# Performance work log

Hardware: AMD Instinct MI355X
Metric: run time of the kernel (lower is better)

## Reference

```python
import jax, jax.numpy as jnp
import numpy as np

HEADS = 8  # init heads


def setup_inputs() -> dict:
    key = jax.random.key(0)
    k1, k2, k3, k4 = jax.random.split(key, 4)
    B, C, L = 32, 512, 32  # batch, dim, lateral_size
    x = jax.random.normal(k1, (B, C, L, L), dtype=jnp.float32)
    # 1x1 conv with no bias == per-pixel matmul; store as [3*dim, dim]
    qkv_w = jax.random.normal(k2, (3 * C, C), dtype=jnp.float32) * (1.0 / np.sqrt(C))
    h_pos = jax.random.normal(k3, (L, 1, C), dtype=jnp.float32) * 0.02
    w_pos = jax.random.normal(k4, (1, L, C), dtype=jnp.float32) * 0.02
    return {"x": x, "qkv_w": qkv_w, "h_pos": h_pos, "w_pos": w_pos}


def reference(x, qkv_w, h_pos, w_pos):
    B, C, H, W = x.shape
    p = HEADS
    d = C // p
    n = H * W
    # QKV 1x1 conv -> [B, 3C, H, W]
    qkv = jnp.einsum('oc,bchw->bohw', qkv_w, x)
    q, k, v = jnp.split(qkv, 3, axis=1)
    # 'b (p d) h w -> b p (h w) d'
    def to_heads(t):
        return t.reshape(B, p, d, H, W).transpose(0, 1, 3, 4, 2).reshape(B, p, n, d)
    q, k, v = to_heads(q), to_heads(k), to_heads(v)
    # relative pos: [H,1,C] + [1,W,C] -> [H,W,C]; 'h w (p d) -> p (h w) d'
    rp = (h_pos + w_pos).reshape(H, W, p, d).transpose(2, 0, 1, 3).reshape(p, n, d)
    # content-position + content-content scores: [B, p, n, n]
    scores = jnp.einsum('bpnd,pmd->bpnm', q, rp) + jnp.einsum('bpnd,bpmd->bpnm', q, k)
    attn = jax.nn.softmax(scores, axis=-1)
    out = jnp.einsum('bpnm,bpmd->bpnd', attn, v)
    # 'b p (h w) d -> b (p d) h w'
    return out.reshape(B, p, H, W, d).transpose(0, 1, 4, 2, 3).reshape(B, C, H, W)
```

## Files before the change

### kernel.cpp

```cpp
#include <hip/hip_runtime.h>
#include <hip/hip_bf16.h>
#include <hip/hip_fp16.h>

#define HEADS 8
#define BB 32
#define CC 512
#define NN 1024
#define DD 64

typedef _Float16 f16;
typedef __attribute__((ext_vector_type(8))) _Float16 f16x8;
typedef __attribute__((ext_vector_type(4))) _Float16 f16x4;
typedef __attribute__((ext_vector_type(2))) __fp16 hf16x2;
typedef __attribute__((ext_vector_type(4))) float f32x4;

__global__ __launch_bounds__(256) void wconv(
    const float* __restrict__ W, f16* __restrict__ Wh)
{
    const size_t i = ((size_t)blockIdx.x * 256 + threadIdx.x) * 8;
    float4 a = *(const float4*)(W + i);
    float4 b = *(const float4*)(W + i + 4);
    f16x8 h = {(f16)a.x, (f16)a.y, (f16)a.z, (f16)a.w,
               (f16)b.x, (f16)b.y, (f16)b.z, (f16)b.w};
    *(f16x8*)(Wh + i) = h;
}

__global__ __launch_bounds__(256) void prep_x(
    const float* __restrict__ x, f16* __restrict__ xt)
{
    __shared__ f16 T[64][65];
    const int tid = threadIdx.x;
    const int c0 = blockIdx.x * 64;
    const int m0 = blockIdx.y * 64;
    const int b  = blockIdx.z;
    const float* xb = x + (size_t)b * CC * NN;

    const int m_l = tid & 63, c_l = tid >> 6;
    #pragma unroll
    for (int s = 0; s < 16; ++s) {
        const int cr = s * 4 + c_l;
        T[cr][m_l] = (f16)xb[(size_t)(c0 + cr) * NN + m0 + m_l];
    }
    __syncthreads();
    const int m_r = tid >> 2, cq = (tid & 3) * 16;
    f16 buf[16];
    #pragma unroll
    for (int j = 0; j < 16; ++j) buf[j] = T[cq + j][m_r];
    f16* dst = xt + ((size_t)b * NN + m0 + m_r) * CC + c0 + cq;
    *(f16x8*)dst       = *(f16x8*)&buf[0];
    *(f16x8*)(dst + 8) = *(f16x8*)&buf[8];
}

#define QST 72

__global__ __launch_bounds__(256) void qkv_mfma(
    const f16*  __restrict__ xt,
    const f16*  __restrict__ Wh,
    const float* __restrict__ h_pos,
    const float* __restrict__ w_pos,
    f16* __restrict__ Qh, f16* __restrict__ Kh, f16* __restrict__ Vt)
{
    __shared__ f16 Xs[128 * QST];
    __shared__ f16 Ws[128 * QST];

    const int tid  = threadIdx.x;
    const int wave = tid >> 6, lane = tid & 63;
    const int ln = lane & 15, quad = lane >> 4;
    const int o0  = blockIdx.x * 128;
    const int mg0 = blockIdx.y * 128;
    const int mw = (wave & 1) * 64, ow = (wave >> 1) * 64;

    f32x4 acc[4][4];
    #pragma unroll
    for (int ia = 0; ia < 4; ++ia)
        #pragma unroll
        for (int ib = 0; ib < 4; ++ib) acc[ia][ib] = (f32x4){0.f, 0.f, 0.f, 0.f};

    const int srow = tid >> 1;
    const int ssub = (tid & 1) * 32;

    for (int ct = 0; ct < 8; ++ct) {
        const int c0 = ct * 64;
        __syncthreads();
        {
            const f16* xg = xt + (size_t)(mg0 + srow) * CC + c0 + ssub;
            const f16* wg = Wh + (size_t)(o0 + srow) * CC + c0 + ssub;
            #pragma unroll
            for (int i = 0; i < 4; ++i) {
                *(f16x8*)&Xs[srow * QST + ssub + i * 8] = *(const f16x8*)(xg + i * 8);
                *(f16x8*)&Ws[srow * QST + ssub + i * 8] = *(const f16x8*)(wg + i * 8);
            }
        }
        __syncthreads();
        #pragma unroll
        for (int ks = 0; ks < 2; ++ks) {
            f16x8 a[4], bf[4];
            #pragma unroll
            for (int f = 0; f < 4; ++f) {
                a[f]  = *(const f16x8*)&Xs[(mw + f * 16 + ln) * QST + ks * 32 + quad * 8];
                bf[f] = *(const f16x8*)&Ws[(ow + f * 16 + ln) * QST + ks * 32 + quad * 8];
            }
            #pragma unroll
            for (int ia = 0; ia < 4; ++ia)
                #pragma unroll
                for (int ib = 0; ib < 4; ++ib)
                    acc[ia][ib] = __builtin_amdgcn_mfma_f32_16x16x32_f16(
                        a[ia], bf[ib], acc[ia][ib], 0, 0, 0);
        }
    }

    const int region = o0 >> 9;
    const int ob = o0 + ow;
    const int p  = (ob >> 6) & 7;
    const int b  = mg0 >> 10;
    const int n0 = (mg0 & 1023) + mw;

    if (region < 2) {
        f16* dst = (region == 0) ? Qh : Kh;
        const size_t hb = (size_t)(b * HEADS + p) * NN * DD;
        #pragma unroll
        for (int ib = 0; ib < 4; ++ib) {
            const int d = ib * 16 + ln;
            #pragma unroll
            for (int ia = 0; ia < 4; ++ia) {
                #pragma unroll
                for (int r = 0; r < 4; ++r) {
                    const int n = n0 + ia * 16 + quad * 4 + r;
                    float v = acc[ia][ib][r];
                    if (region == 1) {
                        const int c = p * DD + d;
                        v += h_pos[(n >> 5) * CC + c] + w_pos[(n & 31) * CC + c];
                    }
                    dst[hb + (size_t)n * DD + d] = (f16)v;
                }
            }
        }
    } else {
        const size_t vb = (size_t)(b * HEADS + p) * DD * NN;
        #pragma unroll
        for (int ib = 0; ib < 4; ++ib) {
            const int d = ib * 16 + ln;
            #pragma unroll
            for (int ia = 0; ia < 4; ++ia) {
                const int n = n0 + ia * 16 + quad * 4;
                f16x4 pk = {(f16)acc[ia][ib][0], (f16)acc[ia][ib][1],
                            (f16)acc[ia][ib][2], (f16)acc[ia][ib][3]};
                *(f16x4*)&Vt[vb + (size_t)d * NN + n] = pk;
            }
        }
    }
}

#define KST 72

__global__ __launch_bounds__(256) void attn_kernel(
    const f16* __restrict__ Qh, const f16* __restrict__ Kh,
    const f16* __restrict__ Vt, float* __restrict__ out)
{
    __shared__ f16 KS [64 * KST];
    __shared__ f16 VtS[64 * KST];
    __shared__ f16 PS [4][16 * KST];

    const int tid  = threadIdx.x;
    const int wave = tid >> 6;
    const int lane = tid & 63;
    const int ln   = lane & 15;
    const int quad = lane >> 4;

    const int qt = blockIdx.x;
    const int p  = blockIdx.y;
    const int b  = blockIdx.z;
    const size_t hb = (size_t)(b * HEADS + p) * NN * DD;

    const int qrow = qt * 64 + wave * 16 + ln;
    f16x8 qf[2];
    #pragma unroll
    for (int ks = 0; ks < 2; ++ks)
        qf[ks] = *(const f16x8*)(Qh + hb + (size_t)qrow * DD + ks * 32 + quad * 8);

    f32x4 o[4];
    #pragma unroll
    for (int dt = 0; dt < 4; ++dt) o[dt] = (f32x4){0.f, 0.f, 0.f, 0.f};
    float lrun = 0.f;
    float mrun = -__builtin_inff();

    const int sr = tid >> 2, sc = (tid & 3) * 16;

    f16x8 kreg0, kreg1, vreg0, vreg1;
    {
        const size_t gk = hb + (size_t)sr * DD + sc;
        kreg0 = *(const f16x8*)(Kh + gk);
        kreg1 = *(const f16x8*)(Kh + gk + 8);
        const size_t gv = hb + (size_t)sr * NN + sc;
        vreg0 = *(const f16x8*)(Vt + gv);
        vreg1 = *(const f16x8*)(Vt + gv + 8);
    }

    f16* Pw = &PS[wave][0];

    for (int kt = 0; kt < 16; ++kt) {
        __syncthreads();
        *(f16x8*)&KS [sr * KST + sc]     = kreg0;
        *(f16x8*)&KS [sr * KST + sc + 8] = kreg1;
        *(f16x8*)&VtS[sr * KST + sc]     = vreg0;
        *(f16x8*)&VtS[sr * KST + sc + 8] = vreg1;
        if (kt < 15) {
            const size_t gk = hb + (size_t)((kt + 1) * 64 + sr) * DD + sc;
            kreg0 = *(const f16x8*)(Kh + gk);
            kreg1 = *(const f16x8*)(Kh + gk + 8);
            const size_t gv = hb + (size_t)sr * NN + (kt + 1) * 64 + sc;
            vreg0 = *(const f16x8*)(Vt + gv);
            vreg1 = *(const f16x8*)(Vt + gv + 8);
        }
        __syncthreads();

        f32x4 s[4];
        #pragma unroll
        for (int nt = 0; nt < 4; ++nt) s[nt] = (f32x4){0.f, 0.f, 0.f, 0.f};
        #pragma unroll
        for (int ks = 0; ks < 2; ++ks) {
            #pragma unroll
            for (int nt = 0; nt < 4; ++nt) {
                f16x8 bk = *(const f16x8*)&KS[(nt * 16 + ln) * KST + ks * 32 + quad * 8];
                s[nt] = __builtin_amdgcn_mfma_f32_16x16x32_f16(bk, qf[ks], s[nt], 0, 0, 0);
            }
        }

        float mx = s[0][0];
        #pragma unroll
        for (int nt = 0; nt < 4; ++nt)
            #pragma unroll
            for (int r = 0; r < 4; ++r) mx = fmaxf(mx, s[nt][r]);
        mx = fmaxf(mx, __shfl_xor(mx, 16));
        mx = fmaxf(mx, __shfl_xor(mx, 32));
        const float mnew = fmaxf(mrun, mx);
        const float alpha = __expf(mrun - mnew);
        mrun = mnew;

        float lsum = 0.f;
        #pragma unroll
        for (int nt = 0; nt < 4; ++nt) {
            const float p0 = __expf(s[nt][0] - mrun);
            const float p1 = __expf(s[nt][1] - mrun);
            const float p2 = __expf(s[nt][2] - mrun);
            const float p3 = __expf(s[nt][3] - mrun);
            lsum += (p0 + p1) + (p2 + p3);
            hf16x2 lo = __builtin_amdgcn_cvt_pkrtz(p0, p1);
            hf16x2 hi = __builtin_amdgcn_cvt_pkrtz(p2, p3);
            f16x4 pk = {(f16)lo.x, (f16)lo.y, (f16)hi.x, (f16)hi.y};
            *(f16x4*)&Pw[ln * KST + nt * 16 + quad * 4] = pk;
        }
        lsum += __shfl_xor(lsum, 16);
        lsum += __shfl_xor(lsum, 32);
        lrun = lrun * alpha + lsum;

        #pragma unroll
        for (int dt = 0; dt < 4; ++dt) {
            o[dt][0] *= alpha; o[dt][1] *= alpha;
            o[dt][2] *= alpha; o[dt][3] *= alpha;
        }

        asm volatile("s_waitcnt lgkmcnt(0)" ::: "memory");

        #pragma unroll
        for (int ks = 0; ks < 2; ++ks) {
            f16x8 pa = *(const f16x8*)&Pw[ln * KST + ks * 32 + quad * 8];
            #pragma unroll
            for (int dt = 0; dt < 4; ++dt) {
                f16x8 vb = *(const f16x8*)&VtS[(dt * 16 + ln) * KST + ks * 32 + quad * 8];
                o[dt] = __builtin_amdgcn_mfma_f32_16x16x32_f16(vb, pa, o[dt], 0, 0, 0);
            }
        }
    }

    const float inv = 1.0f / lrun;
    const int nq = qt * 64 + wave * 16 + ln;
    #pragma unroll
    for (int dt = 0; dt < 4; ++dt) {
        const int c = p * DD + dt * 16 + quad * 4;
        #pragma unroll
        for (int r = 0; r < 4; ++r)
            out[((size_t)b * CC + c + r) * NN + nq] = o[dt][r] * inv;
    }
}

extern "C" void kernel_launch(void* const* d_in, const int* in_sizes, int n_in,
                              void* d_out, int out_size, void* d_ws, size_t ws_size,
                              hipStream_t stream) {
    const float* x     = (const float*)d_in[0];
    const float* qkv_w = (const float*)d_in[1];
    const float* h_pos = (const float*)d_in[2];
    const float* w_pos = (const float*)d_in[3];
    float* out = (float*)d_out;

    const size_t PT = (size_t)BB * HEADS * NN * DD;
    f16* xt = (f16*)d_ws;
    f16* Qh = xt + PT;
    f16* Kh = Qh + PT;
    f16* Vt = Kh + PT;
    f16* Wh = Vt + PT;

    wconv<<<dim3(3 * CC * CC / (256 * 8)), 256, 0, stream>>>(qkv_w, Wh);
    prep_x<<<dim3(CC / 64, NN / 64, BB), 256, 0, stream>>>(x, xt);
    qkv_mfma<<<dim3(12, 256), 256, 0, stream>>>(xt, Wh, h_pos, w_pos, Qh, Kh, Vt);
    attn_kernel<<<dim3(16, HEADS, BB), 256, 0, stream>>>(Qh, Kh, Vt, out);
}
```

Measured before the change: 384.3 us.

## Use direct global-to-LDS loads in QKV GEMM and XCD-aware block swizzling

New measurement: 381.2 us. Within noise of the previous version (-0.8%).

```diff
diff --git a/kernel.cpp b/kernel.cpp
--- a/kernel.cpp
+++ b/kernel.cpp
@@ -13,6 +13,12 @@
 typedef __attribute__((ext_vector_type(4))) _Float16 f16x4;
 typedef __attribute__((ext_vector_type(2))) __fp16 hf16x2;
 typedef __attribute__((ext_vector_type(4))) float f32x4;
+
+__device__ __forceinline__ void gload16(const f16* g, f16* l) {
+    __builtin_amdgcn_global_load_lds(
+        (const __attribute__((address_space(1))) void*)g,
+        (__attribute__((address_space(3))) void*)l, 16, 0, 0);
+}
 
 __global__ __launch_bounds__(256) void wconv(
     const float* __restrict__ W, f16* __restrict__ Wh)
@@ -51,8 +57,6 @@
     *(f16x8*)(dst + 8) = *(f16x8*)&buf[8];
 }
 
-#define QST 72
-
 __global__ __launch_bounds__(256) void qkv_mfma(
     const f16*  __restrict__ xt,
     const f16*  __restrict__ Wh,
@@ -60,14 +64,20 @@
     const float* __restrict__ w_pos,
     f16* __restrict__ Qh, f16* __restrict__ Kh, f16* __restrict__ Vt)
 {
-    __shared__ f16 Xs[128 * QST];
-    __shared__ f16 Ws[128 * QST];
+    __shared__ f16 Xs[128 * 64];
+    __shared__ f16 Ws[128 * 64];
 
     const int tid  = threadIdx.x;
     const int wave = tid >> 6, lane = tid & 63;
     const int ln = lane & 15, quad = lane >> 4;
-    const int o0  = blockIdx.x * 128;
-    const int mg0 = blockIdx.y * 128;
+
+    const unsigned bid  = blockIdx.x;
+    const unsigned xcd  = bid & 7;
+    const unsigned slot = bid >> 3;
+    const unsigned ot   = slot % 12u;
+    const unsigned mt   = xcd * 32u + slot / 12u;
+    const int o0  = (int)ot * 128;
+    const int mg0 = (int)mt * 128;
     const int mw = (wave & 1) * 64, ow = (wave >> 1) * 64;
 
     f32x4 acc[4][4];
@@ -76,20 +86,20 @@
         #pragma unroll
         for (int ib = 0; ib < 4; ++ib) acc[ia][ib] = (f32x4){0.f, 0.f, 0.f, 0.f};
 
-    const int srow = tid >> 1;
-    const int ssub = (tid & 1) * 32;
+    const int sr = wave * 32 + (lane >> 3);
+    const int sc = (lane & 7) * 8;
+    const f16* xg = xt + (size_t)(mg0 + sr) * CC + sc;
+    const f16* wg = Wh + (size_t)(o0  + sr) * CC + sc;
+    f16* xl = &Xs[(wave * 32) * 64];
+    f16* wl = &Ws[(wave * 32) * 64];
 
     for (int ct = 0; ct < 8; ++ct) {
         const int c0 = ct * 64;
         __syncthreads();
-        {
-            const f16* xg = xt + (size_t)(mg0 + srow) * CC + c0 + ssub;
-            const f16* wg = Wh + (size_t)(o0 + srow) * CC + c0 + ssub;
-            #pragma unroll
-            for (int i = 0; i < 4; ++i) {
-                *(f16x8*)&Xs[srow * QST + ssub + i * 8] = *(const f16x8*)(xg + i * 8);
-                *(f16x8*)&Ws[srow * QST + ssub + i * 8] = *(const f16x8*)(wg + i * 8);
-            }
+        #pragma unroll
+        for (int i = 0; i < 4; ++i) {
+            gload16(xg + (size_t)i * 8 * CC + c0, xl + i * 8 * 64);
+            gload16(wg + (size_t)i * 8 * CC + c0, wl + i * 8 * 64);
         }
         __syncthreads();
         #pragma unroll
@@ -97,8 +107,8 @@
             f16x8 a[4], bf[4];
             #pragma unroll
             for (int f = 0; f < 4; ++f) {
-                a[f]  = *(const f16x8*)&Xs[(mw + f * 16 + ln) * QST + ks * 32 + quad * 8];
-                bf[f] = *(const f16x8*)&Ws[(ow + f * 16 + ln) * QST + ks * 32 + quad * 8];
+                a[f]  = *(const f16x8*)&Xs[(mw + f * 16 + ln) * 64 + ks * 32 + quad * 8];
+                bf[f] = *(const f16x8*)&Ws[(ow + f * 16 + ln) * 64 + ks * 32 + quad * 8];
             }
             #pragma unroll
             for (int ia = 0; ia < 4; ++ia)
@@ -167,9 +177,13 @@
     const int ln   = lane & 15;
     const int quad = lane >> 4;
 
-    const int qt = blockIdx.x;
-    const int p  = blockIdx.y;
-    const int b  = blockIdx.z;
+    const unsigned bid  = blockIdx.x;
+    const unsigned xcd  = bid & 7;
+    const unsigned slot = bid >> 3;
+    const int qt = (int)(slot & 15u);
+    const unsigned g = xcd * 32u + (slot >> 4);
+    const int b = (int)(g >> 3);
+    const int p = (int)(g & 7u);
     const size_t hb = (size_t)(b * HEADS + p) * NN * DD;
 
     const int qrow = qt * 64 + wave * 16 + ln;
@@ -302,6 +316,6 @@
 
     wconv<<<dim3(3 * CC * CC / (256 * 8)), 256, 0, stream>>>(qkv_w, Wh);
     prep_x<<<dim3(CC / 64, NN / 64, BB), 256, 0, stream>>>(x, xt);
-    qkv_mfma<<<dim3(12, 256), 256, 0, stream>>>(xt, Wh, h_pos, w_pos, Qh, Kh, Vt);
-    attn_kernel<<<dim3(16, HEADS, BB), 256, 0, stream>>>(Qh, Kh, Vt, out);
-}
+    qkv_mfma<<<dim3(3072), 256, 0, stream>>>(xt, Wh, h_pos, w_pos, Qh, Kh, Vt);
+    attn_kernel<<<dim3(4096), 256, 0, stream>>>(Qh, Kh, Vt, out);
+}
```
